# Kernel tuning notes

Measured on AMD Instinct MI355X. Metric: run time of the kernel, lower is better.

Reference implementation:

```python
import jax, jax.numpy as jnp
import numpy as np

D = 512    # d_model == EMBED_DIM
H = 8      # nhead
FF = 2048  # dim_feedforward
T, B, S, M = 64, 32, 64, 256
EPS = 1e-5


def setup_inputs() -> dict:
    key = jax.random.key(0)
    ks = iter(jax.random.split(key, 40))
    rn = lambda k, shp, s=0.02: s * jax.random.normal(k, shp, jnp.float32)
    inp = {
        'tgt': jax.random.normal(next(ks), (T, B, D), jnp.float32),
        'memory': jax.random.normal(next(ks), (M, B, D), jnp.float32),
        'semantics': jax.random.normal(next(ks), (B, S, D), jnp.float32),
    }
    for pfx in ('pt', 'sa', 'ca'):  # pre_target, self_attn, cross multihead_attn
        inp[pfx + '_wqkv'] = rn(next(ks), (3 * D, D))
        inp[pfx + '_bqkv'] = jnp.zeros((3 * D,), jnp.float32)
        inp[pfx + '_wo'] = rn(next(ks), (D, D))
        inp[pfx + '_bo'] = jnp.zeros((D,), jnp.float32)
    # relevant_mlp_pre_target: fc0 (2D->D), relu, fc1 (D->D), relu, fc2 (D->1)
    inp['mlp_w0'] = rn(next(ks), (D, 2 * D), float(np.sqrt(2.0 / (2 * D))))
    inp['mlp_b0'] = jnp.zeros((D,), jnp.float32)
    inp['mlp_w1'] = rn(next(ks), (D, D), float(np.sqrt(2.0 / D)))
    inp['mlp_b1'] = jnp.zeros((D,), jnp.float32)
    inp['mlp_w2'] = rn(next(ks), (1, D), float(np.sqrt(2.0 / D)))
    inp['mlp_b2'] = jnp.zeros((1,), jnp.float32)
    inp['ffn_w1'] = rn(next(ks), (FF, D))
    inp['ffn_b1'] = jnp.zeros((FF,), jnp.float32)
    inp['ffn_w2'] = rn(next(ks), (D, FF))
    inp['ffn_b2'] = jnp.zeros((D,), jnp.float32)
    for i in (1, 2, 3):
        inp[f'ln{i}_g'] = jnp.ones((D,), jnp.float32)
        inp[f'ln{i}_b'] = jnp.zeros((D,), jnp.float32)
    return inp


def layernorm(x, g, b):
    mu = jnp.mean(x, -1, keepdims=True)
    var = jnp.var(x, -1, keepdims=True)
    return (x - mu) * jax.lax.rsqrt(var + EPS) * g + b


def mha(q, k, v, wqkv, bqkv, wo, bo):
    # q,k,v: (L, B, D) seq-first, like torch nn.MultiheadAttention
    hd = D // H
    wq, wk, wv = jnp.split(wqkv, 3, axis=0)
    bq, bk, bv = jnp.split(bqkv, 3)
    qh = (q @ wq.T + bq).reshape(q.shape[0], q.shape[1], H, hd)
    kh = (k @ wk.T + bk).reshape(k.shape[0], k.shape[1], H, hd)
    vh = (v @ wv.T + bv).reshape(v.shape[0], v.shape[1], H, hd)
    scale = 1.0 / float(np.sqrt(hd))
    att = jax.nn.softmax(jnp.einsum('qbhd,kbhd->bhqk', qh * scale, kh), axis=-1)
    out = jnp.einsum('bhqk,kbhd->qbhd', att, vh).reshape(q.shape[0], q.shape[1], D)
    return out @ wo.T + bo


def get_relevant_semantic(feats, sem, w0, b0, w1, b1, w2, b2):
    # feats: (B,T,D), sem: (B,S,D). Linear-on-concat == sum of two linears, so we
    # never materialize the (B,T,S,2D) cat tensor; hidden (B,T,S,D) is unavoidable math.
    w0c, w0s = w0[:, :D], w0[:, D:]
    h = (feats @ w0c.T)[:, :, None, :] + (sem @ w0s.T)[:, None, :, :] + b0  # (B,T,S,D)
    h = jax.nn.relu(h)
    h = jax.nn.relu(h @ w1.T + b1)
    scores = h @ w2.T + b2                      # (B,T,S,1)
    a = jax.nn.softmax(scores, axis=2)          # softmax over sem axis
    return jnp.sum(sem[:, None, :, :] * a, axis=2)  # (B,T,D)


def reference(tgt, memory, semantics,
              pt_wqkv, pt_bqkv, pt_wo, pt_bo,
              sa_wqkv, sa_bqkv, sa_wo, sa_bo,
              ca_wqkv, ca_bqkv, ca_wo, ca_bo,
              mlp_w0, mlp_b0, mlp_w1, mlp_b1, mlp_w2, mlp_b2,
              ffn_w1, ffn_b1, ffn_w2, ffn_b2,
              ln1_g, ln1_b, ln2_g, ln2_b, ln3_g, ln3_b):
    # MULTIHEAD_PRE_TARGET branch (eval mode: dropout = identity)
    rel = get_relevant_semantic(jnp.transpose(tgt, (1, 0, 2)), semantics,
                                mlp_w0, mlp_b0, mlp_w1, mlp_b1, mlp_w2, mlp_b2)
    sem_k = jnp.transpose(rel, (1, 0, 2))  # (T,B,D) seq-first key/value
    x = tgt + mha(tgt, sem_k, sem_k, pt_wqkv, pt_bqkv, pt_wo, pt_bo)
    # self attention
    x = layernorm(x + mha(x, x, x, sa_wqkv, sa_bqkv, sa_wo, sa_bo), ln1_g, ln1_b)
    # cross attention over encoder memory
    x = layernorm(x + mha(x, memory, memory, ca_wqkv, ca_bqkv, ca_wo, ca_bo), ln2_g, ln2_b)
    # feed-forward
    ff = jax.nn.relu(x @ ffn_w1.T + ffn_b1) @ ffn_w2.T + ffn_b2
    return layernorm(x + ff, ln3_g, ln3_b)
```

## Files before the change

### kernel.cpp

```cpp
#include <hip/hip_runtime.h>
#include <hip/hip_bf16.h>

#define WS_B 32
#define WS_T 64
#define WS_S 64
#define WS_D 512

typedef __attribute__((ext_vector_type(8))) __bf16 bf16x8;
typedef __attribute__((ext_vector_type(4))) float f32x4;
typedef unsigned short ushort_t;

#define MB(x) ((size_t)(x) << 20)

__device__ __forceinline__ unsigned packpair(float lo, float hi) {
    return ((__float_as_uint(lo) + 0x8000u) >> 16) |
           ((__float_as_uint(hi) + 0x8000u) & 0xffff0000u);
}
__device__ __forceinline__ ushort_t f2bf(float x) {
    return (ushort_t)((__float_as_uint(x) + 0x8000u) >> 16);
}
__device__ __forceinline__ float bf2f(ushort_t u) {
    return __uint_as_float(((unsigned)u) << 16);
}
__device__ __forceinline__ unsigned fuse_word(unsigned f, unsigned s) {
    float lo = __uint_as_float(f << 16) + __uint_as_float(s << 16);
    float hi = __uint_as_float(f & 0xffff0000u) + __uint_as_float(s & 0xffff0000u);
    lo = fmaxf(lo, 0.f);
    hi = fmaxf(hi, 0.f);
    return packpair(lo, hi);
}
__device__ __forceinline__ void gl2lds16(const void* g, void* l) {
    __builtin_amdgcn_global_load_lds(
        (const __attribute__((address_space(1))) void*)g,
        (__attribute__((address_space(3))) void*)l, 16, 0, 0);
}

struct CvtArgs {
    const float* src[13];
    ushort_t* dst[13];
    int n4[13];
};
__global__ __launch_bounds__(256) void megacvt_kernel(CvtArgs a) {
    const int t = blockIdx.y;
    const int n = a.n4[t];
    const float4* S = (const float4*)a.src[t];
    uint2* D = (uint2*)a.dst[t];
    for (int i = blockIdx.x * 256 + threadIdx.x; i < n; i += gridDim.x * 256) {
        float4 v = S[i];
        uint2 o;
        o.x = packpair(v.x, v.y);
        o.y = packpair(v.z, v.w);
        D[i] = o;
    }
}

struct GemmDesc {
    const ushort_t* A;
    const ushort_t* W;
    const float* bias;
    const float* resid;
    float* C;
    ushort_t* Cb;
    int lda, ldw, ldc, K, relu, nbx, blkStart;
};
struct GemmBatch {
    GemmDesc d[4];
    int nd;
};

__global__ __launch_bounds__(512, 2) void mfma_gemm_b(GemmBatch bt) {
    __shared__ ushort_t As[128 * 32];
    __shared__ ushort_t Bs[256 * 32];
    int di = 0;
#pragma unroll
    for (int i = 1; i < 4; ++i)
        if (i < bt.nd && (int)blockIdx.x >= bt.d[i].blkStart) di = i;
    const GemmDesc g = bt.d[di];
    const int local = blockIdx.x - g.blkStart;
    const int mb = local / g.nbx;
    const int nb = local - mb * g.nbx;

    const int tid = threadIdx.x;
    const int w = tid >> 6, lane = tid & 63;
    const int wm = w & 1, wn = w >> 1;
    const int l15 = lane & 15, quad = lane >> 4;

    const ushort_t* Ap  = g.A + (long)(mb * 128 + (tid >> 2)) * g.lda + (tid & 3) * 8;
    const ushort_t* Bp0 = g.W + (long)(nb * 256 + (tid >> 2)) * g.ldw + (tid & 3) * 8;
    const ushort_t* Bp1 = Bp0 + (long)128 * g.ldw;
    ushort_t* AsD  = As + w * 512;
    ushort_t* BsD0 = Bs + w * 512;
    ushort_t* BsD1 = Bs + 4096 + w * 512;

    f32x4 acc[4][4];
#pragma unroll
    for (int i = 0; i < 4; ++i)
#pragma unroll
        for (int j = 0; j < 4; ++j) acc[i][j] = (f32x4)0.f;

    for (int k0 = 0; k0 < g.K; k0 += 32) {
        __syncthreads();
        gl2lds16(Ap + k0, AsD);
        gl2lds16(Bp0 + k0, BsD0);
        gl2lds16(Bp1 + k0, BsD1);
        __syncthreads();
        bf16x8 af[4], bf[4];
#pragma unroll
        for (int mt = 0; mt < 4; ++mt)
            af[mt] = *(const bf16x8*)&As[(wm * 64 + mt * 16 + l15) * 32 + quad * 8];
#pragma unroll
        for (int nt = 0; nt < 4; ++nt)
            bf[nt] = *(const bf16x8*)&Bs[(wn * 64 + nt * 16 + l15) * 32 + quad * 8];
#pragma unroll
        for (int mt = 0; mt < 4; ++mt)
#pragma unroll
            for (int nt = 0; nt < 4; ++nt)
                acc[mt][nt] = __builtin_amdgcn_mfma_f32_16x16x32_bf16(
                    af[mt], bf[nt], acc[mt][nt], 0, 0, 0);
    }

#pragma unroll
    for (int nt = 0; nt < 4; ++nt) {
        const int col = nb * 256 + wn * 64 + nt * 16 + l15;
        const float bv = g.bias ? g.bias[col] : 0.f;
#pragma unroll
        for (int mt = 0; mt < 4; ++mt) {
            const int row0 = mb * 128 + wm * 64 + mt * 16 + quad * 4;
#pragma unroll
            for (int rg = 0; rg < 4; ++rg) {
                float v = acc[mt][nt][rg] + bv;
                if (g.relu) v = fmaxf(v, 0.f);
                const long off = (long)(row0 + rg) * g.ldc + col;
                if (g.resid) v += g.resid[off];
                if (g.C) g.C[off] = v;
                if (g.Cb) g.Cb[off] = f2bf(v);
            }
        }
    }
}

__global__ __launch_bounds__(512, 2) void h2score_kernel(
    const ushort_t* __restrict__ Fb,
    const ushort_t* __restrict__ Sb,
    const ushort_t* __restrict__ w1b,
    const float* __restrict__ b1,
    const float* __restrict__ w2,
    float* __restrict__ scores4)
{
    __shared__ ushort_t As[128 * 32];
    __shared__ ushort_t Bs[256 * 32];
    __shared__ float scred[128 * 4];
    const int tid = threadIdx.x;
    const int mb = blockIdx.x, nb = blockIdx.y;
    const int w = tid >> 6, lane = tid & 63;
    const int wm = w & 1, wn = w >> 1;
    const int l15 = lane & 15, quad = lane >> 4;

    const int arow = tid >> 2, akc = tid & 3;
    const int m_g = mb * 128 + arow;
    const int r = m_g >> 6, s = m_g & 63, bidx = r & 31;
    const ushort_t* Fp = Fb + (long)r * 512 + akc * 8;
    const ushort_t* Sp = Sb + (long)(bidx * 64 + s) * 512 + akc * 8;
    const ushort_t* Bp0 = w1b + (long)(nb * 256 + (tid >> 2)) * 512 + (tid & 3) * 8;
    const ushort_t* Bp1 = Bp0 + (long)128 * 512;
    ushort_t* Asw = &As[arow * 32 + akc * 8];
    ushort_t* BsD0 = Bs + w * 512;
    ushort_t* BsD1 = Bs + 4096 + w * 512;

    f32x4 acc[4][4];
#pragma unroll
    for (int i = 0; i < 4; ++i)
#pragma unroll
        for (int j = 0; j < 4; ++j) acc[i][j] = (f32x4)0.f;

    uint4 fa = *(const uint4*)(Fp);
    uint4 sa = *(const uint4*)(Sp);
    for (int k0 = 0; k0 < 512; k0 += 32) {
        __syncthreads();
        gl2lds16(Bp0 + k0, BsD0);
        gl2lds16(Bp1 + k0, BsD1);
        uint4 o;
        o.x = fuse_word(fa.x, sa.x);
        o.y = fuse_word(fa.y, sa.y);
        o.z = fuse_word(fa.z, sa.z);
        o.w = fuse_word(fa.w, sa.w);
        *(uint4*)Asw = o;
        if (k0 + 32 < 512) {
            fa = *(const uint4*)(Fp + k0 + 32);
            sa = *(const uint4*)(Sp + k0 + 32);
        }
        __syncthreads();
        bf16x8 af[4], bf[4];
#pragma unroll
        for (int mt = 0; mt < 4; ++mt)
            af[mt] = *(const bf16x8*)&As[(wm * 64 + mt * 16 + l15) * 32 + quad * 8];
#pragma unroll
        for (int nt = 0; nt < 4; ++nt)
            bf[nt] = *(const bf16x8*)&Bs[(wn * 64 + nt * 16 + l15) * 32 + quad * 8];
#pragma unroll
        for (int mt = 0; mt < 4; ++mt)
#pragma unroll
            for (int nt = 0; nt < 4; ++nt)
                acc[mt][nt] = __builtin_amdgcn_mfma_f32_16x16x32_bf16(
                    af[mt], bf[nt], acc[mt][nt], 0, 0, 0);
    }
    __syncthreads();

    float sp[4][4];
#pragma unroll
    for (int mt = 0; mt < 4; ++mt)
#pragma unroll
        for (int rg = 0; rg < 4; ++rg) sp[mt][rg] = 0.f;
#pragma unroll
    for (int nt = 0; nt < 4; ++nt) {
        const int col = nb * 256 + wn * 64 + nt * 16 + l15;
        const float cb = b1[col];
        const float cw = w2[col];
#pragma unroll
        for (int mt = 0; mt < 4; ++mt) {
#pragma unroll
            for (int rg = 0; rg < 4; ++rg)
                sp[mt][rg] += fmaxf(acc[mt][nt][rg] + cb, 0.f) * cw;
        }
    }
#pragma unroll
    for (int mt = 0; mt < 4; ++mt)
#pragma unroll
        for (int rg = 0; rg < 4; ++rg) {
            float v = sp[mt][rg];
            v += __shfl_xor(v, 1);
            v += __shfl_xor(v, 2);
            v += __shfl_xor(v, 4);
            v += __shfl_xor(v, 8);
            if (l15 == 0)
                scred[(wm * 64 + mt * 16 + quad * 4 + rg) * 4 + wn] = v;
        }
    __syncthreads();
    if (tid < 128) {
        float t = scred[tid * 4] + scred[tid * 4 + 1]
                + scred[tid * 4 + 2] + scred[tid * 4 + 3];
        scores4[(long)nb * 131072 + mb * 128 + tid] = t;
    }
}

__global__ __launch_bounds__(256) void softrel_kernel(
    const float* __restrict__ sc4,
    const float* __restrict__ sem,
    ushort_t* __restrict__ rel)
{
    __shared__ float a_s[64];
    const int tid = threadIdx.x;
    const int r = blockIdx.x;
    const int b = r & (WS_B - 1);
    if (tid < 64) {
        float t = sc4[r * 64 + tid] + sc4[131072 + r * 64 + tid];
        float m = t;
#pragma unroll
        for (int off = 32; off > 0; off >>= 1) m = fmaxf(m, __shfl_xor(m, off));
        float e = __expf(t - m);
        float su = e;
#pragma unroll
        for (int off = 32; off > 0; off >>= 1) su += __shfl_xor(su, off);
        a_s[tid] = e / su;
    }
    __syncthreads();
#pragma unroll
    for (int dd = 0; dd < 2; ++dd) {
        const int d = tid + dd * 256;
        float accd = 0.f;
        const float* sp = sem + (long)b * 64 * 512 + d;
        for (int s = 0; s < 64; ++s)
            accd += a_s[s] * sp[s * 512];
        rel[(long)r * 512 + d] = f2bf(accd);
    }
}

__global__ __launch_bounds__(256) void attn2_kernel(
    const ushort_t* __restrict__ Qm, int ldq, int qoff,
    const ushort_t* __restrict__ Km, int ldk, int koff,
    const ushort_t* __restrict__ Vm, int ldv, int voff,
    ushort_t* __restrict__ O,
    int Lk)
{
    __shared__ float sQT[64 * 34];
    __shared__ float sKT[64 * 68];
    __shared__ float sS[32 * 260];
    __shared__ float sredm[8 * 34];
    __shared__ float sreds[8 * 34];
    const int tid = threadIdx.x;
    const int b  = blockIdx.x >> 4;
    const int h  = (blockIdx.x >> 1) & 7;
    const int qt = blockIdx.x & 1;
    const int L8 = Lk >> 3;

    {
        const int q = tid >> 3, c = tid & 7;
        const int qg = qt * 32 + q;
        const ushort_t* pp = Qm + (long)(qg * WS_B + b) * ldq + qoff + h * 64 + c * 8;
        uint4 u = *(const uint4*)pp;
        const ushort_t* us = (const ushort_t*)&u;
#pragma unroll
        for (int i = 0; i < 8; ++i)
            sQT[(c * 8 + i) * 34 + q] = bf2f(us[i]);
    }

    const int k4 = (tid & 15) * 4;
    const int q2 = (tid >> 4) * 2;

    for (int kt = 0; kt < Lk; kt += 64) {
        __syncthreads();
        {
            const int kk = tid >> 3, c = tid & 7;
#pragma unroll
            for (int half = 0; half < 2; ++half) {
                const int kr = kk + half * 32;
                const ushort_t* pp = Km + (long)((kt + kr) * WS_B + b) * ldk + koff + h * 64 + c * 8;
                uint4 u = *(const uint4*)pp;
                const ushort_t* us = (const ushort_t*)&u;
#pragma unroll
                for (int i = 0; i < 8; ++i)
                    sKT[(c * 8 + i) * 68 + kr] = bf2f(us[i]);
            }
        }
        __syncthreads();
        float acc[2][4] = {{0.f, 0.f, 0.f, 0.f}, {0.f, 0.f, 0.f, 0.f}};
        for (int d = 0; d < 64; ++d) {
            const float qa = sQT[d * 34 + q2];
            const float qb = sQT[d * 34 + q2 + 1];
            const float4 kv = *(const float4*)&sKT[d * 68 + k4];
            acc[0][0] += qa * kv.x; acc[0][1] += qa * kv.y;
            acc[0][2] += qa * kv.z; acc[0][3] += qa * kv.w;
            acc[1][0] += qb * kv.x; acc[1][1] += qb * kv.y;
            acc[1][2] += qb * kv.z; acc[1][3] += qb * kv.w;
        }
#pragma unroll
        for (int i = 0; i < 2; ++i) {
            float4 v;
            v.x = acc[i][0] * 0.125f; v.y = acc[i][1] * 0.125f;
            v.z = acc[i][2] * 0.125f; v.w = acc[i][3] * 0.125f;
            *(float4*)&sS[(q2 + i) * 260 + kt + k4] = v;
        }
    }
    __syncthreads();

    {
        const int q = tid & 31, part = tid >> 5;
        const int kb = part * L8;
        float m = -1e30f;
        for (int k = 0; k < L8; ++k) m = fmaxf(m, sS[q * 260 + kb + k]);
        sredm[part * 34 + q] = m;
        __syncthreads();
        float M = sredm[q];
#pragma unroll
        for (int pz = 1; pz < 8; ++pz) M = fmaxf(M, sredm[pz * 34 + q]);
        float su = 0.f;
        for (int k = 0; k < L8; ++k) {
            float e = __expf(sS[q * 260 + kb + k] - M);
            sS[q * 260 + kb + k] = e;
            su += e;
        }
        sreds[part * 34 + q] = su;
    }
    __syncthreads();

    const int d4 = (tid & 15) * 4;
    float o[2][4] = {{0.f, 0.f, 0.f, 0.f}, {0.f, 0.f, 0.f, 0.f}};
    float* sV = sKT;
    for (int kt = 0; kt < Lk; kt += 64) {
        __syncthreads();
        {
            const int kk = tid >> 3, c = tid & 7;
#pragma unroll
            for (int half = 0; half < 2; ++half) {
                const int kr = kk + half * 32;
                const ushort_t* pp = Vm + (long)((kt + kr) * WS_B + b) * ldv + voff + h * 64 + c * 8;
                uint4 u = *(const uint4*)pp;
                const ushort_t* us = (const ushort_t*)&u;
                float4 w0, w1;
                w0.x = bf2f(us[0]); w0.y = bf2f(us[1]);
                w0.z = bf2f(us[2]); w0.w = bf2f(us[3]);
                w1.x = bf2f(us[4]); w1.y = bf2f(us[5]);
                w1.z = bf2f(us[6]); w1.w = bf2f(us[7]);
                *(float4*)&sV[kr * 68 + c * 8] = w0;
                *(float4*)&sV[kr * 68 + c * 8 + 4] = w1;
            }
        }
        __syncthreads();
        for (int k = 0; k < 64; ++k) {
            const float p0 = sS[q2 * 260 + kt + k];
            const float p1 = sS[(q2 + 1) * 260 + kt + k];
            const float4 vv = *(const float4*)&sV[k * 68 + d4];
            o[0][0] += p0 * vv.x; o[0][1] += p0 * vv.y;
            o[0][2] += p0 * vv.z; o[0][3] += p0 * vv.w;
            o[1][0] += p1 * vv.x; o[1][1] += p1 * vv.y;
            o[1][2] += p1 * vv.z; o[1][3] += p1 * vv.w;
        }
    }

#pragma unroll
    for (int i = 0; i < 2; ++i) {
        float su = 0.f;
#pragma unroll
        for (int pz = 0; pz < 8; ++pz) su += sreds[pz * 34 + q2 + i];
        const float inv = 1.f / su;
        const int qg = qt * 32 + q2 + i;
        ushort_t* op = O + (long)(qg * WS_B + b) * 512 + h * 64 + d4;
        uint2 pk;
        pk.x = packpair(o[i][0] * inv, o[i][1] * inv);
        pk.y = packpair(o[i][2] * inv, o[i][3] * inv);
        *(uint2*)op = pk;
    }
}

__global__ __launch_bounds__(256) void ln_kernel(
    const float* __restrict__ X,
    const float* __restrict__ g,
    const float* __restrict__ be,
    float* __restrict__ Y,
    ushort_t* __restrict__ Yb)
{
    const int row = blockIdx.x * 4 + (threadIdx.x >> 6);
    const int lane = threadIdx.x & 63;
    const float4* xp = (const float4*)(X + (long)row * WS_D);
    float4 x0 = xp[lane], x1 = xp[lane + 64];
    float sum = x0.x + x0.y + x0.z + x0.w + x1.x + x1.y + x1.z + x1.w;
    float sq = x0.x * x0.x + x0.y * x0.y + x0.z * x0.z + x0.w * x0.w
             + x1.x * x1.x + x1.y * x1.y + x1.z * x1.z + x1.w * x1.w;
#pragma unroll
    for (int off = 32; off > 0; off >>= 1) {
        sum += __shfl_xor(sum, off);
        sq += __shfl_xor(sq, off);
    }
    const float mu = sum * (1.f / 512.f);
    const float var = sq * (1.f / 512.f) - mu * mu;
    const float rs = rsqrtf(var + 1e-5f);
    const float4* gp = (const float4*)g;
    const float4* bp = (const float4*)be;
    float4 g0 = gp[lane], g1 = gp[lane + 64], b0 = bp[lane], b1 = bp[lane + 64];
    float4 y0, y1;
    y0.x = (x0.x - mu) * rs * g0.x + b0.x;
    y0.y = (x0.y - mu) * rs * g0.y + b0.y;
    y0.z = (x0.z - mu) * rs * g0.z + b0.z;
    y0.w = (x0.w - mu) * rs * g0.w + b0.w;
    y1.x = (x1.x - mu) * rs * g1.x + b1.x;
    y1.y = (x1.y - mu) * rs * g1.y + b1.y;
    y1.z = (x1.z - mu) * rs * g1.z + b1.z;
    y1.w = (x1.w - mu) * rs * g1.w + b1.w;
    float4* yp = (float4*)(Y + (long)row * WS_D);
    yp[lane] = y0; yp[lane + 64] = y1;
    if (Yb) {
        uint2* ybp = (uint2*)(Yb + (long)row * WS_D);
        uint2 p0, p1;
        p0.x = packpair(y0.x, y0.y); p0.y = packpair(y0.z, y0.w);
        p1.x = packpair(y1.x, y1.y); p1.y = packpair(y1.z, y1.w);
        ybp[lane] = p0; ybp[lane + 64] = p1;
    }
}

static inline GemmDesc mkdesc(const ushort_t* A, int lda, const ushort_t* W, int ldw,
                              const float* bias, const float* resid, float* C,
                              ushort_t* Cb, int ldc, int N, int K, int relu,
                              int blkStart)
{
    GemmDesc d;
    d.A = A; d.W = W; d.bias = bias; d.resid = resid; d.C = C; d.Cb = Cb;
    d.lda = lda; d.ldw = ldw; d.ldc = ldc; d.K = K; d.relu = relu;
    d.nbx = N / 256;
    d.blkStart = blkStart;
    return d;
}
static inline void mgemm(hipStream_t s, const ushort_t* A, int lda,
                         const ushort_t* W, int ldw, const float* bias,
                         const float* resid, float* C, ushort_t* Cb,
                         int ldc, int M, int N, int K, bool relu)
{
    GemmBatch bt;
    bt.nd = 1;
    bt.d[0] = mkdesc(A, lda, W, ldw, bias, resid, C, Cb, ldc, N, K, relu ? 1 : 0, 0);
    bt.d[1] = bt.d[0]; bt.d[2] = bt.d[0]; bt.d[3] = bt.d[0];
    mfma_gemm_b<<<(M / 128) * (N / 256), 512, 0, s>>>(bt);
}

extern "C" void kernel_launch(void* const* d_in, const int* in_sizes, int n_in,
                              void* d_out, int out_size, void* d_ws, size_t ws_size,
                              hipStream_t stream)
{
    (void)in_sizes; (void)n_in; (void)out_size; (void)ws_size;
    const float* tgt       = (const float*)d_in[0];
    const float* memory    = (const float*)d_in[1];
    const float* semantics = (const float*)d_in[2];
    const float* pt_wqkv   = (const float*)d_in[3];
    const float* pt_bqkv   = (const float*)d_in[4];
    const float* pt_wo     = (const float*)d_in[5];
    const float* pt_bo     = (const float*)d_in[6];
    const float* sa_wqkv   = (const float*)d_in[7];
    const float* sa_bqkv   = (const float*)d_in[8];
    const float* sa_wo     = (const float*)d_in[9];
    const float* sa_bo     = (const float*)d_in[10];
    const float* ca_wqkv   = (const float*)d_in[11];
    const float* ca_bqkv   = (const float*)d_in[12];
    const float* ca_wo     = (const float*)d_in[13];
    const float* ca_bo     = (const float*)d_in[14];
    const float* mlp_w0    = (const float*)d_in[15];
    const float* mlp_b0    = (const float*)d_in[16];
    const float* mlp_w1    = (const float*)d_in[17];
    const float* mlp_b1    = (const float*)d_in[18];
    const float* mlp_w2    = (const float*)d_in[19];
    const float* ffn_w1    = (const float*)d_in[21];
    const float* ffn_b1    = (const float*)d_in[22];
    const float* ffn_w2    = (const float*)d_in[23];
    const float* ffn_b2    = (const float*)d_in[24];
    const float* ln1_g     = (const float*)d_in[25];
    const float* ln1_b     = (const float*)d_in[26];
    const float* ln2_g     = (const float*)d_in[27];
    const float* ln2_b     = (const float*)d_in[28];
    const float* ln3_g     = (const float*)d_in[29];
    const float* ln3_b     = (const float*)d_in[30];

    char* p = (char*)d_ws;
    ushort_t* w0b   = (ushort_t*)(p + 0);
    ushort_t* w1b   = (ushort_t*)(p + MB(1));
    ushort_t* ptwb  = (ushort_t*)(p + 1572864);
    ushort_t* ptob  = (ushort_t*)(p + MB(3));
    ushort_t* sawb  = (ushort_t*)(p + 3670016);
    ushort_t* saob  = (ushort_t*)(p + MB(5));
    ushort_t* cawb  = (ushort_t*)(p + 5767168);
    ushort_t* caob  = (ushort_t*)(p + MB(7));
    ushort_t* f1b   = (ushort_t*)(p + 7864320);
    ushort_t* f2b   = (ushort_t*)(p + 9961472);
    ushort_t* memb  = (ushort_t*)(p + MB(12));
    ushort_t* cakvb = (ushort_t*)(p + MB(20));
    ushort_t* tgtb  = (ushort_t*)(p + MB(36));
    ushort_t* semb  = (ushort_t*)(p + MB(38));
    ushort_t* Fb    = (ushort_t*)(p + MB(40));
    ushort_t* Sb    = (ushort_t*)(p + MB(42));
    float*    scores4 = (float*)(p + MB(44));
    ushort_t* relb  = (ushort_t*)(p + MB(45));
    ushort_t* Ob    = (ushort_t*)(p + MB(47));
    float*    x1f   = (float*)(p + MB(49));
    ushort_t* ptqb  = (ushort_t*)(p + MB(53));
    ushort_t* ptkvb = (ushort_t*)(p + MB(14));
    ushort_t* x1b   = (ushort_t*)(p + MB(18));
    ushort_t* saqkvb= (ushort_t*)(p + MB(38));
    float*    yf    = (float*)(p + MB(12));
    float*    x2f   = (float*)(p + MB(16));
    ushort_t* x2b   = (ushort_t*)(p + MB(36));
    ushort_t* caqb  = (ushort_t*)(p + MB(44));
    float*    x3f   = (float*)(p + MB(40));
    ushort_t* x3b   = (ushort_t*)(p + MB(38));
    ushort_t* hb    = (ushort_t*)(p + MB(20));

    CvtArgs ca;
    ca.src[0]  = tgt;       ca.dst[0]  = tgtb;  ca.n4[0]  = 262144;
    ca.src[1]  = semantics; ca.dst[1]  = semb;  ca.n4[1]  = 262144;
    ca.src[2]  = memory;    ca.dst[2]  = memb;  ca.n4[2]  = 1048576;
    ca.src[3]  = mlp_w0;    ca.dst[3]  = w0b;   ca.n4[3]  = 131072;
    ca.src[4]  = mlp_w1;    ca.dst[4]  = w1b;   ca.n4[4]  = 65536;
    ca.src[5]  = pt_wqkv;   ca.dst[5]  = ptwb;  ca.n4[5]  = 196608;
    ca.src[6]  = pt_wo;     ca.dst[6]  = ptob;  ca.n4[6]  = 65536;
    ca.src[7]  = sa_wqkv;   ca.dst[7]  = sawb;  ca.n4[7]  = 196608;
    ca.src[8]  = sa_wo;     ca.dst[8]  = saob;  ca.n4[8]  = 65536;
    ca.src[9]  = ca_wqkv;   ca.dst[9]  = cawb;  ca.n4[9]  = 196608;
    ca.src[10] = ca_wo;     ca.dst[10] = caob;  ca.n4[10] = 65536;
    ca.src[11] = ffn_w1;    ca.dst[11] = f1b;   ca.n4[11] = 262144;
    ca.src[12] = ffn_w2;    ca.dst[12] = f2b;   ca.n4[12] = 262144;
    megacvt_kernel<<<dim3(1024, 13), 256, 0, stream>>>(ca);

    {
        GemmBatch bt;
        bt.nd = 4;
        bt.d[0] = mkdesc(memb, 512, cawb + 512 * 512, 512, ca_bqkv + 512, nullptr,
                         nullptr, cakvb, 1024, 1024, 512, 0, 0);
        bt.d[1] = mkdesc(tgtb, 512, w0b, 1024, mlp_b0, nullptr,
                         nullptr, Fb, 512, 512, 512, 0, 256);
        bt.d[2] = mkdesc(semb, 512, w0b + 512, 1024, nullptr, nullptr,
                         nullptr, Sb, 512, 512, 512, 0, 288);
        bt.d[3] = mkdesc(tgtb, 512, ptwb, 512, pt_bqkv, nullptr,
                         nullptr, ptqb, 512, 512, 512, 0, 320);
        mfma_gemm_b<<<352, 512, 0, stream>>>(bt);
    }

    h2score_kernel<<<dim3(1024, 2), 512, 0, stream>>>(Fb, Sb, w1b, mlp_b1,
                                                      mlp_w2, scores4);
    softrel_kernel<<<2048, 256, 0, stream>>>(scores4, semantics, relb);

    mgemm(stream, relb, 512, ptwb + 512 * 512, 512, pt_bqkv + 512, nullptr,
          nullptr, ptkvb, 1024, 2048, 1024, 512, false);
    attn2_kernel<<<512, 256, 0, stream>>>(ptqb, 512, 0, ptkvb, 1024, 0,
                                          ptkvb, 1024, 512, Ob, 64);
    mgemm(stream, Ob, 512, ptob, 512, pt_bo, tgt, x1f, x1b, 512,
          2048, 512, 512, false);

    mgemm(stream, x1b, 512, sawb, 512, sa_bqkv, nullptr, nullptr, saqkvb, 1536,
          2048, 1536, 512, false);
    attn2_kernel<<<512, 256, 0, stream>>>(saqkvb, 1536, 0, saqkvb, 1536, 512,
                                          saqkvb, 1536, 1024, Ob, 64);
    mgemm(stream, Ob, 512, saob, 512, sa_bo, x1f, yf, nullptr, 512,
          2048, 512, 512, false);
    ln_kernel<<<512, 256, 0, stream>>>(yf, ln1_g, ln1_b, x2f, x2b);

    mgemm(stream, x2b, 512, cawb, 512, ca_bqkv, nullptr, nullptr, caqb, 512,
          2048, 512, 512, false);
    attn2_kernel<<<512, 256, 0, stream>>>(caqb, 512, 0, cakvb, 1024, 0,
                                          cakvb, 1024, 512, Ob, 256);
    mgemm(stream, Ob, 512, caob, 512, ca_bo, x2f, yf, nullptr, 512,
          2048, 512, 512, false);
    ln_kernel<<<512, 256, 0, stream>>>(yf, ln2_g, ln2_b, x3f, x3b);

    mgemm(stream, x3b, 512, f1b, 512, ffn_b1, nullptr, nullptr, hb, 2048,
          2048, 2048, 512, true);
    mgemm(stream, hb, 2048, f2b, 2048, ffn_b2, x3f, yf, nullptr, 512,
          2048, 512, 2048, false);
    ln_kernel<<<512, 256, 0, stream>>>(yf, ln3_g, ln3_b, (float*)d_out, nullptr);
}
```

Baseline: 612.5 us.

## Shrink GEMM tile to 128x128, pad LDS rows, register-prefetch loads, bf16 semantics in softrel

Replaces the 512-thread 128x256 GEMM with a 256-thread 128x128 tile kernel that prefetches the next K-slice into registers and writes it to LDS with a padded row stride of 40 to avoid bank conflicts. The direct global-to-LDS loads are dropped in both the GEMM and the h2score kernel in favour of register staging. The score kernel now reads the bf16 copy of semantics instead of fp32, halving that read traffic at a small precision cost. Smaller tiles double the block count for more occupancy on small GEMMs but reduce per-block reuse of the loaded weights.

```diff
diff --git a/kernel.cpp b/kernel.cpp
--- a/kernel.cpp
+++ b/kernel.cpp
@@ -2,15 +2,13 @@
 #include <hip/hip_bf16.h>
 
 #define WS_B 32
-#define WS_T 64
-#define WS_S 64
-#define WS_D 512
 
 typedef __attribute__((ext_vector_type(8))) __bf16 bf16x8;
 typedef __attribute__((ext_vector_type(4))) float f32x4;
 typedef unsigned short ushort_t;
 
 #define MB(x) ((size_t)(x) << 20)
+#define LSTR 40
 
 __device__ __forceinline__ unsigned packpair(float lo, float hi) {
     return ((__float_as_uint(lo) + 0x8000u) >> 16) |
@@ -28,11 +26,6 @@
     lo = fmaxf(lo, 0.f);
     hi = fmaxf(hi, 0.f);
     return packpair(lo, hi);
-}
-__device__ __forceinline__ void gl2lds16(const void* g, void* l) {
-    __builtin_amdgcn_global_load_lds(
-        (const __attribute__((address_space(1))) void*)g,
-        (__attribute__((address_space(3))) void*)l, 16, 0, 0);
 }
 
 struct CvtArgs {
@@ -68,9 +61,9 @@
     int nd;
 };
 
-__global__ __launch_bounds__(512, 2) void mfma_gemm_b(GemmBatch bt) {
-    __shared__ ushort_t As[128 * 32];
-    __shared__ ushort_t Bs[256 * 32];
+__global__ __launch_bounds__(256, 3) void mfma_gemm2(GemmBatch bt) {
+    __shared__ ushort_t As[128 * LSTR];
+    __shared__ ushort_t Bs[128 * LSTR];
     int di = 0;
 #pragma unroll
     for (int i = 1; i < 4; ++i)
@@ -85,12 +78,12 @@
     const int wm = w & 1, wn = w >> 1;
     const int l15 = lane & 15, quad = lane >> 4;
 
-    const ushort_t* Ap  = g.A + (long)(mb * 128 + (tid >> 2)) * g.lda + (tid & 3) * 8;
-    const ushort_t* Bp0 = g.W + (long)(nb * 256 + (tid >> 2)) * g.ldw + (tid & 3) * 8;
-    const ushort_t* Bp1 = Bp0 + (long)128 * g.ldw;
-    ushort_t* AsD  = As + w * 512;
-    ushort_t* BsD0 = Bs + w * 512;
-    ushort_t* BsD1 = Bs + 4096 + w * 512;
+    const int arow = tid >> 1;
+    const int a16 = (tid & 1) * 16;
+    const ushort_t* Ap = g.A + (long)(mb * 128 + arow) * g.lda + a16;
+    const ushort_t* Bp = g.W + (long)(nb * 128 + arow) * g.ldw + a16;
+    ushort_t* Asw = &As[arow * LSTR + a16];
+    ushort_t* Bsw = &Bs[arow * LSTR + a16];
 
     f32x4 acc[4][4];
 #pragma unroll
@@ -98,19 +91,29 @@
 #pragma unroll
         for (int j = 0; j < 4; ++j) acc[i][j] = (f32x4)0.f;
 
+    uint4 a0 = *(const uint4*)Ap;
+    uint4 a1 = *(const uint4*)(Ap + 8);
+    uint4 b0 = *(const uint4*)Bp;
+    uint4 b1 = *(const uint4*)(Bp + 8);
+
     for (int k0 = 0; k0 < g.K; k0 += 32) {
         __syncthreads();
-        gl2lds16(Ap + k0, AsD);
-        gl2lds16(Bp0 + k0, BsD0);
-        gl2lds16(Bp1 + k0, BsD1);
+        *(uint4*)Asw = a0; *(uint4*)(Asw + 8) = a1;
+        *(uint4*)Bsw = b0; *(uint4*)(Bsw + 8) = b1;
+        if (k0 + 32 < g.K) {
+            a0 = *(const uint4*)(Ap + k0 + 32);
+            a1 = *(const uint4*)(Ap + k0 + 40);
+            b0 = *(const uint4*)(Bp + k0 + 32);
+            b1 = *(const uint4*)(Bp + k0 + 40);
+        }
         __syncthreads();
         bf16x8 af[4], bf[4];
 #pragma unroll
         for (int mt = 0; mt < 4; ++mt)
-            af[mt] = *(const bf16x8*)&As[(wm * 64 + mt * 16 + l15) * 32 + quad * 8];
+            af[mt] = *(const bf16x8*)&As[(wm * 64 + mt * 16 + l15) * LSTR + quad * 8];
 #pragma unroll
         for (int nt = 0; nt < 4; ++nt)
-            bf[nt] = *(const bf16x8*)&Bs[(wn * 64 + nt * 16 + l15) * 32 + quad * 8];
+            bf[nt] = *(const bf16x8*)&Bs[(wn * 64 + nt * 16 + l15) * LSTR + quad * 8];
 #pragma unroll
         for (int mt = 0; mt < 4; ++mt)
 #pragma unroll
@@ -121,7 +124,7 @@
 
 #pragma unroll
     for (int nt = 0; nt < 4; ++nt) {
-        const int col = nb * 256 + wn * 64 + nt * 16 + l15;
+        const int col = nb * 128 + wn * 64 + nt * 16 + l15;
         const float bv = g.bias ? g.bias[col] : 0.f;
 #pragma unroll
         for (int mt = 0; mt < 4; ++mt) {
@@ -147,8 +150,8 @@
     const float* __restrict__ w2,
     float* __restrict__ scores4)
 {
-    __shared__ ushort_t As[128 * 32];
-    __shared__ ushort_t Bs[256 * 32];
+    __shared__ ushort_t As[128 * LSTR];
+    __shared__ ushort_t Bs[256 * LSTR];
     __shared__ float scred[128 * 4];
     const int tid = threadIdx.x;
     const int mb = blockIdx.x, nb = blockIdx.y;
@@ -161,11 +164,11 @@
     const int r = m_g >> 6, s = m_g & 63, bidx = r & 31;
     const ushort_t* Fp = Fb + (long)r * 512 + akc * 8;
     const ushort_t* Sp = Sb + (long)(bidx * 64 + s) * 512 + akc * 8;
-    const ushort_t* Bp0 = w1b + (long)(nb * 256 + (tid >> 2)) * 512 + (tid & 3) * 8;
+    const ushort_t* Bp0 = w1b + (long)(nb * 256 + arow) * 512 + akc * 8;
     const ushort_t* Bp1 = Bp0 + (long)128 * 512;
-    ushort_t* Asw = &As[arow * 32 + akc * 8];
-    ushort_t* BsD0 = Bs + w * 512;
-    ushort_t* BsD1 = Bs + 4096 + w * 512;
+    ushort_t* Asw  = &As[arow * LSTR + akc * 8];
+    ushort_t* Bsw0 = &Bs[arow * LSTR + akc * 8];
+    ushort_t* Bsw1 = Bsw0 + 128 * LSTR;
 
     f32x4 acc[4][4];
 #pragma unroll
@@ -173,30 +176,35 @@
 #pragma unroll
         for (int j = 0; j < 4; ++j) acc[i][j] = (f32x4)0.f;
 
-    uint4 fa = *(const uint4*)(Fp);
-    uint4 sa = *(const uint4*)(Sp);
+    uint4 fa = *(const uint4*)Fp;
+    uint4 sa = *(const uint4*)Sp;
+    uint4 bb0 = *(const uint4*)Bp0;
+    uint4 bb1 = *(const uint4*)Bp1;
+
     for (int k0 = 0; k0 < 512; k0 += 32) {
         __syncthreads();
-        gl2lds16(Bp0 + k0, BsD0);
-        gl2lds16(Bp1 + k0, BsD1);
         uint4 o;
         o.x = fuse_word(fa.x, sa.x);
         o.y = fuse_word(fa.y, sa.y);
         o.z = fuse_word(fa.z, sa.z);
         o.w = fuse_word(fa.w, sa.w);
         *(uint4*)Asw = o;
+        *(uint4*)Bsw0 = bb0;
+        *(uint4*)Bsw1 = bb1;
         if (k0 + 32 < 512) {
-            fa = *(const uint4*)(Fp + k0 + 32);
-            sa = *(const uint4*)(Sp + k0 + 32);
+            fa  = *(const uint4*)(Fp + k0 + 32);
+            sa  = *(const uint4*)(Sp + k0 + 32);
+            bb0 = *(const uint4*)(Bp0 + k0 + 32);
+            bb1 = *(const uint4*)(Bp1 + k0 + 32);
         }
         __syncthreads();
         bf16x8 af[4], bf[4];
 #pragma unroll
         for (int mt = 0; mt < 4; ++mt)
-            af[mt] = *(const bf16x8*)&As[(wm * 64 + mt * 16 + l15) * 32 + quad * 8];
+            af[mt] = *(const bf16x8*)&As[(wm * 64 + mt * 16 + l15) * LSTR + quad * 8];
 #pragma unroll
         for (int nt = 0; nt < 4; ++nt)
-            bf[nt] = *(const bf16x8*)&Bs[(wn * 64 + nt * 16 + l15) * 32 + quad * 8];
+            bf[nt] = *(const bf16x8*)&Bs[(wn * 64 + nt * 16 + l15) * LSTR + quad * 8];
 #pragma unroll
         for (int mt = 0; mt < 4; ++mt)
 #pragma unroll
@@ -245,7 +253,7 @@
 
 __global__ __launch_bounds__(256) void softrel_kernel(
     const float* __restrict__ sc4,
-    const float* __restrict__ sem,
+    const ushort_t* __restrict__ semb,
     ushort_t* __restrict__ rel)
 {
     __shared__ float a_s[64];
@@ -268,9 +276,9 @@
     for (int dd = 0; dd < 2; ++dd) {
         const int d = tid + dd * 256;
         float accd = 0.f;
-        const float* sp = sem + (long)b * 64 * 512 + d;
+        const ushort_t* sp = semb + (long)b * 64 * 512 + d;
         for (int s = 0; s < 64; ++s)
-            accd += a_s[s] * sp[s * 512];
+            accd += a_s[s] * bf2f(sp[s * 512]);
         rel[(long)r * 512 + d] = f2bf(accd);
     }
 }
@@ -421,7 +429,7 @@
 {
     const int row = blockIdx.x * 4 + (threadIdx.x >> 6);
     const int lane = threadIdx.x & 63;
-    const float4* xp = (const float4*)(X + (long)row * WS_D);
+    const float4* xp = (const float4*)(X + (long)row * 512);
     float4 x0 = xp[lane], x1 = xp[lane + 64];
     float sum = x0.x + x0.y + x0.z + x0.w + x1.x + x1.y + x1.z + x1.w;
     float sq = x0.x * x0.x + x0.y * x0.y + x0.z * x0.z + x0.w * x0.w
@@ -446,10 +454,10 @@
     y1.y = (x1.y - mu) * rs * g1.y + b1.y;
     y1.z = (x1.z - mu) * rs * g1.z + b1.z;
     y1.w = (x1.w - mu) * rs * g1.w + b1.w;
-    float4* yp = (float4*)(Y + (long)row * WS_D);
+    float4* yp = (float4*)(Y + (long)row * 512);
     yp[lane] = y0; yp[lane + 64] = y1;
     if (Yb) {
-        uint2* ybp = (uint2*)(Yb + (long)row * WS_D);
+        uint2* ybp = (uint2*)(Yb + (long)row * 512);
         uint2 p0, p1;
         p0.x = packpair(y0.x, y0.y); p0.y = packpair(y0.z, y0.w);
         p1.x = packpair(y1.x, y1.y); p1.y = packpair(y1.z, y1.w);
@@ -465,7 +473,7 @@
     GemmDesc d;
     d.A = A; d.W = W; d.bias = bias; d.resid = resid; d.C = C; d.Cb = Cb;
     d.lda = lda; d.ldw = ldw; d.ldc = ldc; d.K = K; d.relu = relu;
-    d.nbx = N / 256;
+    d.nbx = N / 128;
     d.blkStart = blkStart;
     return d;
 }
@@ -478,7 +486,7 @@
     bt.nd = 1;
     bt.d[0] = mkdesc(A, lda, W, ldw, bias, resid, C, Cb, ldc, N, K, relu ? 1 : 0, 0);
     bt.d[1] = bt.d[0]; bt.d[2] = bt.d[0]; bt.d[3] = bt.d[0];
-    mfma_gemm_b<<<(M / 128) * (N / 256), 512, 0, s>>>(bt);
+    mfma_gemm2<<<(M / 128) * (N / 128), 256, 0, s>>>(bt);
 }
 
 extern "C" void kernel_launch(void* const* d_in, const int* in_sizes, int n_in,
@@ -572,17 +580,17 @@
         bt.d[0] = mkdesc(memb, 512, cawb + 512 * 512, 512, ca_bqkv + 512, nullptr,
                          nullptr, cakvb, 1024, 1024, 512, 0, 0);
         bt.d[1] = mkdesc(tgtb, 512, w0b, 1024, mlp_b0, nullptr,
-                         nullptr, Fb, 512, 512, 512, 0, 256);
+                         nullptr, Fb, 512, 512, 512, 0, 512);
         bt.d[2] = mkdesc(semb, 512, w0b + 512, 1024, nullptr, nullptr,
-                         nullptr, Sb, 512, 512, 512, 0, 288);
+                         nullptr, Sb, 512, 512, 512, 0, 576);
         bt.d[3] = mkdesc(tgtb, 512, ptwb, 512, pt_bqkv, nullptr,
-                         nullptr, ptqb, 512, 512, 512, 0, 320);
-        mfma_gemm_b<<<352, 512, 0, stream>>>(bt);
+                         nullptr, ptqb, 512, 512, 512, 0, 640);
+        mfma_gemm2<<<704, 256, 0, stream>>>(bt);
     }
 
     h2score_kernel<<<dim3(1024, 2), 512, 0, stream>>>(Fb, Sb, w1b, mlp_b1,
                                                       mlp_w2, scores4);
-    softrel_kernel<<<2048, 256, 0, stream>>>(scores4, semantics, relb);
+    softrel_kernel<<<2048, 256, 0, stream>>>(scores4, semb, relb);
 
     mgemm(stream, relb, 512, ptwb + 512 * 512, 512, pt_bqkv + 512, nullptr,
           nullptr, ptkvb, 1024, 2048, 1024, 512, false);
```

Result: faster. 527.7 us (-13.9%).
